# Optimization experiments

Hardware: AMD Instinct MI355X
Metric: run time of the kernel (lower is better)

## Reference

```python
import jax, jax.numpy as jnp
import numpy as np
from jax import lax


def setup_inputs() -> dict:
    key = jax.random.key(0)
    k1, k2, k3, k4, k5 = jax.random.split(key, 5)
    B, T, V, E, U = 64, 256, 32000, 256, 1024
    x = jax.random.randint(k1, (B, T), 0, V)          # token ids; 0 = pad (mask_zero=True)
    hidden = jnp.zeros((B, U), dtype=jnp.float32)      # initialize_hidden_state()
    emb = jax.random.normal(k2, (V, E), dtype=jnp.float32) * 0.05
    W = jax.random.normal(k3, (E, 3 * U), dtype=jnp.float32) * 0.05   # input kernel [z|r|h]
    Uk = jax.random.normal(k4, (U, 3 * U), dtype=jnp.float32) * 0.05  # recurrent kernel
    b = jax.random.normal(k5, (2, 3 * U), dtype=jnp.float32) * 0.05   # [input_bias, recurrent_bias] (reset_after=True)
    return {"x": x, "hidden": hidden, "emb": emb, "W": W, "U": Uk, "b": b}


def reference(x, hidden, emb, W, U, b):
    # Embedding with mask_zero=True: mask out pad tokens in the GRU scan.
    mask = (x != 0)                              # [B, T] bool
    xe = emb[x]                                  # [B, T, E]
    # Precompute all input projections in one big GEMM.
    xproj = jnp.einsum("bte,eu->btu", xe, W) + b[0]   # [B, T, 3U]
    nU = U.shape[0]

    def step(h, inp):
        xp, m = inp                              # xp: [B, 3U], m: [B]
        rec = h @ U + b[1]                       # [B, 3U]
        xz, xr, xh = jnp.split(xp, 3, axis=-1)
        rz, rr, rh = jnp.split(rec, 3, axis=-1)
        z = jax.nn.sigmoid(xz + rz)
        r = jax.nn.sigmoid(xr + rr)
        hh = jnp.tanh(xh + r * rh)               # reset_after=True form
        h_new = z * h + (1.0 - z) * hh
        h_new = jnp.where(m[:, None], h_new, h)  # masked steps carry state/output through
        return h_new, h_new

    state, outs = lax.scan(step, hidden,
                           (jnp.swapaxes(xproj, 0, 1), jnp.swapaxes(mask, 0, 1)))
    output = jnp.swapaxes(outs, 0, 1)            # [B, T, U]
    return output, state
```

## Files before the change

kernel.cpp:

```cpp
#include <hip/hip_runtime.h>
#include <hip/hip_cooperative_groups.h>

#define BB 64
#define TT 256
#define EE 256
#define NU 1024
#define N3 3072

typedef __attribute__((ext_vector_type(8))) short bf16x8;
typedef __attribute__((ext_vector_type(4))) float f32x4;

__device__ __forceinline__ unsigned short f2bf(float f) {
    unsigned u = __float_as_uint(f);
    return (unsigned short)((u + 0x7FFFu + ((u >> 16) & 1u)) >> 16);
}

__global__ __launch_bounds__(256) void upack_kernel(
    const float* __restrict__ U, float* __restrict__ up)
{
    __shared__ float t32[32][33];
    const int c0 = blockIdx.x * 32, k0 = blockIdx.y * 32;
    const int tx = threadIdx.x & 31, ty = threadIdx.x >> 5;
    #pragma unroll
    for (int i = 0; i < 4; ++i) {
        int k = ty + i * 8;
        t32[k][tx] = U[(size_t)(k0 + k) * N3 + c0 + tx];
    }
    __syncthreads();
    #pragma unroll
    for (int i = 0; i < 4; ++i) {
        int cl = ty + i * 8;
        int c = c0 + cl;
        int u = c & 1023, g = c >> 10;
        up[(size_t)(u * 3 + g) * NU + k0 + tx] = t32[tx][cl];
    }
}

__global__ __launch_bounds__(64) void tokT_kernel(
    const int* __restrict__ x, int* __restrict__ xT)
{
    const int t = blockIdx.x, b = threadIdx.x;
    xT[t * BB + b] = x[b * TT + t];
}

__global__ __launch_bounds__(256) void hinit_kernel(
    const float* __restrict__ hidden, unsigned short* __restrict__ hb0,
    unsigned* __restrict__ cnt)
{
    const int u = blockIdx.x * 4 + (threadIdx.x >> 6);
    const int b = threadIdx.x & 63;
    hb0[((u >> 3) * 64 + b) * 8 + (u & 7)] = f2bf(hidden[(size_t)b * NU + u]);
    if (blockIdx.x == 0) {
        cnt[threadIdx.x] = 0u;
        cnt[threadIdx.x + 256] = 0u;
    }
}

__global__ __launch_bounds__(256) void xprojT_kernel(
    const int* __restrict__ x, const float* __restrict__ emb,
    const float* __restrict__ W, const float* __restrict__ bias,
    float* __restrict__ xpT)
{
    __shared__ float AsT[32][132];
    __shared__ float Ws[32][132];
    __shared__ int toks[128];

    const int tid = threadIdx.x;
    const int mt = blockIdx.x / 24, nt = blockIdx.x % 24;
    const int m0 = mt * 128, n0 = nt * 128;

    if (tid < 128) {
        int mg = m0 + tid;
        toks[tid] = x[(mg & 63) * TT + (mg >> 6)];
    }
    __syncthreads();

    const int tx = tid & 15, ty = tid >> 4;
    float acc[8][8] = {};

    for (int kb = 0; kb < 8; ++kb) {
        const int k0 = kb * 32;
        if (kb) __syncthreads();
        #pragma unroll
        for (int i = 0; i < 4; ++i) {
            int idx = tid + 256 * i;
            int m = idx >> 3, c4 = idx & 7;
            float4 av = *(const float4*)(emb + (size_t)toks[m] * EE + k0 + c4 * 4);
            AsT[c4 * 4 + 0][m] = av.x; AsT[c4 * 4 + 1][m] = av.y;
            AsT[c4 * 4 + 2][m] = av.z; AsT[c4 * 4 + 3][m] = av.w;
            int r = idx >> 5, w4 = idx & 31;
            *(float4*)&Ws[r][w4 * 4] =
                *(const float4*)(W + (size_t)(k0 + r) * N3 + n0 + w4 * 4);
        }
        __syncthreads();
        #pragma unroll 8
        for (int kk = 0; kk < 32; ++kk) {
            float a8[8], w8[8];
            *(float4*)a8       = *(const float4*)&AsT[kk][ty * 8];
            *(float4*)(a8 + 4) = *(const float4*)&AsT[kk][ty * 8 + 4];
            *(float4*)w8       = *(const float4*)&Ws[kk][tx * 8];
            *(float4*)(w8 + 4) = *(const float4*)&Ws[kk][tx * 8 + 4];
            #pragma unroll
            for (int i = 0; i < 8; ++i)
                #pragma unroll
                for (int j = 0; j < 8; ++j) acc[i][j] += a8[i] * w8[j];
        }
    }

    float b8[8];
    *(float4*)b8       = *(const float4*)(bias + n0 + tx * 8);
    *(float4*)(b8 + 4) = *(const float4*)(bias + n0 + tx * 8 + 4);
    const int t0 = mt * 2 + (ty >> 3);
    const int bb0 = (ty & 7) * 8;
    #pragma unroll
    for (int j = 0; j < 8; ++j) {
        const int c = n0 + tx * 8 + j;
        float4 lo, hi;
        lo.x = acc[0][j] + b8[j]; lo.y = acc[1][j] + b8[j];
        lo.z = acc[2][j] + b8[j]; lo.w = acc[3][j] + b8[j];
        hi.x = acc[4][j] + b8[j]; hi.y = acc[5][j] + b8[j];
        hi.z = acc[6][j] + b8[j]; hi.w = acc[7][j] + b8[j];
        size_t base = ((size_t)t0 * N3 + c) * BB + bb0;
        *(float4*)(xpT + base)     = lo;
        *(float4*)(xpT + base + 4) = hi;
    }
}

__global__ __launch_bounds__(512) void gru_persist(
    const int* __restrict__ xT, const float* __restrict__ upack,
    const float* __restrict__ bias, float* xpT,
    float* __restrict__ out, const float* __restrict__ hidden,
    unsigned short* hb0, unsigned short* hb1, unsigned* cnt)
{
    __shared__ f32x4 red2[6144];
    __shared__ f32x4 redS[768];
    __shared__ unsigned short hstage[64 * 20];

    const int tid = threadIdx.x;
    const int U0 = blockIdx.x * 16;
    const int w = tid >> 6;
    const int lane = tid & 63;

    const int gdu = tid >> 5;
    const int gbA = tid & 31;

    bf16x8 af[3][4];
    {
        const int du = lane & 15;
        #pragma unroll
        for (int g = 0; g < 3; ++g)
            #pragma unroll
            for (int s = 0; s < 4; ++s) {
                const int k0 = w * 128 + s * 32 + (lane >> 4) * 8;
                const float* p = upack + (size_t)((U0 + du) * 3 + g) * NU + k0;
                float4 v0 = *(const float4*)p;
                float4 v1 = *(const float4*)(p + 4);
                af[g][s] = (bf16x8){ (short)f2bf(v0.x), (short)f2bf(v0.y),
                                     (short)f2bf(v0.z), (short)f2bf(v0.w),
                                     (short)f2bf(v1.x), (short)f2bf(v1.y),
                                     (short)f2bf(v1.z), (short)f2bf(v1.w) };
            }
    }

    float holdA = hidden[(size_t)gbA * NU + U0 + gdu];
    float holdB = hidden[(size_t)(gbA + 32) * NU + U0 + gdu];
    const float brz = bias[N3 + 0 * NU + U0 + gdu];
    const float brr = bias[N3 + 1 * NU + U0 + gdu];
    const float brh = bias[N3 + 2 * NU + U0 + gdu];
    float xzA, xrA, xhA, xzB, xrB, xhB; int tokA, tokB;
    {
        size_t xb = ((size_t)0 * N3 + U0 + gdu) * BB + gbA;
        xzA = xpT[xb];                      xzB = xpT[xb + 32];
        xrA = xpT[xb + (size_t)NU * BB];    xrB = xpT[xb + (size_t)NU * BB + 32];
        xhA = xpT[xb + (size_t)2 * NU * BB];xhB = xpT[xb + (size_t)2 * NU * BB + 32];
        tokA = xT[0 * BB + gbA];            tokB = xT[0 * BB + gbA + 32];
    }
    float* state_out = out + (size_t)BB * TT * NU;
    __syncthreads();

    const unsigned short* hc = hb0;
    unsigned short* hn = hb1;

    for (int t = 0; t < TT; ++t) {
        if (t > 0) {
            size_t ob = ((size_t)(t - 1) * N3 + U0 + gdu) * BB + gbA;
            __hip_atomic_store(&xpT[ob], holdA,
                               __ATOMIC_RELAXED, __HIP_MEMORY_SCOPE_SYSTEM);
            __hip_atomic_store(&xpT[ob + 32], holdB,
                               __ATOMIC_RELAXED, __HIP_MEMORY_SCOPE_SYSTEM);
        }

        bf16x8 bv[4][4];
        #pragma unroll
        for (int n = 0; n < 4; ++n)
            #pragma unroll
            for (int s = 0; s < 4; ++s) {
                const int ew = w * 16 + s * 4 + (lane >> 4);
                const unsigned long long* hq = (const unsigned long long*)(hc +
                    (size_t)(ew * 64 + n * 16 + (lane & 15)) * 8);
                union { unsigned long long q[2]; bf16x8 v; } uu;
                uu.q[0] = __hip_atomic_load(hq, __ATOMIC_RELAXED,
                                            __HIP_MEMORY_SCOPE_SYSTEM);
                uu.q[1] = __hip_atomic_load(hq + 1, __ATOMIC_RELAXED,
                                            __HIP_MEMORY_SCOPE_SYSTEM);
                bv[n][s] = uu.v;
            }

        f32x4 c[3][4];
        #pragma unroll
        for (int g = 0; g < 3; ++g)
            #pragma unroll
            for (int n = 0; n < 4; ++n) c[g][n] = (f32x4){0.f, 0.f, 0.f, 0.f};
        #pragma unroll
        for (int s = 0; s < 4; ++s)
            #pragma unroll
            for (int g = 0; g < 3; ++g)
                #pragma unroll
                for (int n = 0; n < 4; ++n)
                    c[g][n] = __builtin_amdgcn_mfma_f32_16x16x32_bf16(
                        af[g][s], bv[n][s], c[g][n], 0, 0, 0);

        #pragma unroll
        for (int g = 0; g < 3; ++g)
            #pragma unroll
            for (int n = 0; n < 4; ++n)
                red2[(w * 12 + g * 4 + n) * 64 + lane] = c[g][n];
        __syncthreads();

        {
            f32x4 s0 = red2[tid];
            #pragma unroll
            for (int q = 1; q < 8; ++q) s0 += red2[q * 768 + tid];
            redS[tid] = s0;
            if (tid < 256) {
                const int o2 = 512 + tid;
                f32x4 s1 = red2[o2];
                #pragma unroll
                for (int q = 1; q < 8; ++q) s1 += red2[q * 768 + o2];
                redS[o2] = s1;
            }
        }
        __syncthreads();

        {
            const int lA = (gdu >> 2) * 16 + (gbA & 15);
            const int rsub = gdu & 3;
            const int nA = gbA >> 4;
            float rzA = brz + ((const float*)&redS[(0 * 4 + nA) * 64 + lA])[rsub];
            float rrA = brr + ((const float*)&redS[(1 * 4 + nA) * 64 + lA])[rsub];
            float rhA = brh + ((const float*)&redS[(2 * 4 + nA) * 64 + lA])[rsub];
            float rzB = brz + ((const float*)&redS[(0 * 4 + nA + 2) * 64 + lA])[rsub];
            float rrB = brr + ((const float*)&redS[(1 * 4 + nA + 2) * 64 + lA])[rsub];
            float rhB = brh + ((const float*)&redS[(2 * 4 + nA + 2) * 64 + lA])[rsub];

            float zA  = 1.f / (1.f + expf(-(xzA + rzA)));
            float rA  = 1.f / (1.f + expf(-(xrA + rrA)));
            float hhA = tanhf(xhA + rA * rhA);
            float hnewA = zA * holdA + (1.f - zA) * hhA;
            if (tokA == 0) hnewA = holdA;
            float zB  = 1.f / (1.f + expf(-(xzB + rzB)));
            float rB  = 1.f / (1.f + expf(-(xrB + rrB)));
            float hhB = tanhf(xhB + rB * rhB);
            float hnewB = zB * holdB + (1.f - zB) * hhB;
            if (tokB == 0) hnewB = holdB;

            hstage[gbA * 20 + gdu] = f2bf(hnewA);
            hstage[(gbA + 32) * 20 + gdu] = f2bf(hnewB);
            holdA = hnewA; holdB = hnewB;
        }
        __syncthreads();

        if (w == 4 || w == 5) {
            const int g2 = w - 4;
            unsigned long long lo =
                *(const unsigned long long*)&hstage[lane * 20 + 8 * g2];
            unsigned long long hi =
                *(const unsigned long long*)&hstage[lane * 20 + 8 * g2 + 4];
            unsigned short* dst = hn + ((size_t)((U0 >> 3) + g2) * 64 + lane) * 8;
            __hip_atomic_store((unsigned long long*)dst, lo,
                               __ATOMIC_RELAXED, __HIP_MEMORY_SCOPE_SYSTEM);
            __hip_atomic_store((unsigned long long*)(dst + 4), hi,
                               __ATOMIC_RELAXED, __HIP_MEMORY_SCOPE_SYSTEM);
        }

        __builtin_amdgcn_s_waitcnt(0);
        __syncthreads();

        if (t + 1 < TT) {
            size_t xb = ((size_t)(t + 1) * N3 + U0 + gdu) * BB + gbA;
            xzA = xpT[xb];                      xzB = xpT[xb + 32];
            xrA = xpT[xb + (size_t)NU * BB];    xrB = xpT[xb + (size_t)NU * BB + 32];
            xhA = xpT[xb + (size_t)2 * NU * BB];xhB = xpT[xb + (size_t)2 * NU * BB + 32];
            tokA = xT[(t + 1) * BB + gbA];      tokB = xT[(t + 1) * BB + gbA + 32];
        }

        if (tid == 0) {
            const unsigned g = (unsigned)blockIdx.x >> 3;
            __hip_atomic_fetch_add(&cnt[g * 32], 1u,
                                   __ATOMIC_RELAXED, __HIP_MEMORY_SCOPE_SYSTEM);
            const unsigned tgt = 8u * ((unsigned)t + 1u);
            unsigned mn;
            long guard = 0;
            do {
                mn = 0xffffffffu;
                #pragma unroll
                for (int g8 = 0; g8 < 8; ++g8) {
                    unsigned v = __hip_atomic_load(&cnt[g8 * 32],
                                  __ATOMIC_RELAXED, __HIP_MEMORY_SCOPE_SYSTEM);
                    mn = v < mn ? v : mn;
                }
                if (mn < tgt) __builtin_amdgcn_s_sleep(1);
            } while (mn < tgt && ++guard < (1L << 24));
        }
        __syncthreads();

        const unsigned short* tmp = hc; hc = hn; hn = (unsigned short*)tmp;
    }

    {
        size_t ob = ((size_t)(TT - 1) * N3 + U0 + gdu) * BB + gbA;
        __hip_atomic_store(&xpT[ob], holdA,
                           __ATOMIC_RELAXED, __HIP_MEMORY_SCOPE_SYSTEM);
        __hip_atomic_store(&xpT[ob + 32], holdB,
                           __ATOMIC_RELAXED, __HIP_MEMORY_SCOPE_SYSTEM);
        __hip_atomic_store(&state_out[(size_t)gbA * NU + U0 + gdu], holdA,
                           __ATOMIC_RELAXED, __HIP_MEMORY_SCOPE_SYSTEM);
        __hip_atomic_store(&state_out[(size_t)(gbA + 32) * NU + U0 + gdu], holdB,
                           __ATOMIC_RELAXED, __HIP_MEMORY_SCOPE_SYSTEM);
    }
}

__global__ __launch_bounds__(256) void outT_kernel(
    const float* __restrict__ xpT, float* __restrict__ out)
{
    __shared__ float tile[64][65];
    const int t = blockIdx.x, u0 = blockIdx.y * 64;
    const int lane = threadIdx.x & 63, row = threadIdx.x >> 6;
    #pragma unroll
    for (int r = row; r < 64; r += 4)
        tile[r][lane] = xpT[((size_t)t * N3 + u0 + r) * BB + lane];
    __syncthreads();
    #pragma unroll
    for (int b = row; b < 64; b += 4)
        out[((size_t)b * TT + t) * NU + u0 + lane] = tile[lane][b];
}

extern "C" void kernel_launch(void* const* d_in, const int* in_sizes, int n_in,
                              void* d_out, int out_size, void* d_ws, size_t ws_size,
                              hipStream_t stream) {
    const int*   x      = (const int*)d_in[0];
    const float* hidden = (const float*)d_in[1];
    const float* emb    = (const float*)d_in[2];
    const float* W      = (const float*)d_in[3];
    const float* U      = (const float*)d_in[4];
    const float* bvec   = (const float*)d_in[5];

    float* out = (float*)d_out;

    float*          xpT   = (float*)d_ws;
    float*          upck  = xpT + (size_t)16384 * N3;
    unsigned short* hb0   = (unsigned short*)(upck + (size_t)3 * NU * NU);
    unsigned short* hb1   = hb0 + (size_t)NU * BB;
    int*            xT    = (int*)(hb1 + (size_t)NU * BB);
    unsigned*       cnt   = (unsigned*)(xT + TT * BB);

    upack_kernel<<<dim3(96, 32), dim3(256), 0, stream>>>(U, upck);
    tokT_kernel<<<dim3(TT), dim3(64), 0, stream>>>(x, xT);
    hinit_kernel<<<dim3(256), dim3(256), 0, stream>>>(hidden, hb0, cnt);
    xprojT_kernel<<<dim3(3072), dim3(256), 0, stream>>>(x, emb, W, bvec, xpT);

    void* args[] = {(void*)&xT, (void*)&upck, (void*)&bvec, (void*)&xpT,
                    (void*)&out, (void*)&hidden, (void*)&hb0, (void*)&hb1,
                    (void*)&cnt};
    hipLaunchCooperativeKernel((const void*)gru_persist, dim3(64), dim3(512),
                               args, 0, stream);

    outT_kernel<<<dim3(TT, 16), dim3(256), 0, stream>>>(xpT, out);
}
```

Measured before the change: 2.135 ms.

## Overlap input-projection GEMM with GRU recurrence inside the persistent kernel

The separate embedding/input-projection GEMM kernel is folded into the cooperative launch as 192 extra producer blocks. These compute xproj tiles and publish per-time-tile ready counters, which the 64 recurrence blocks poll before loading each step's inputs. The recurrence now writes hidden outputs straight into the final output layout, which removes the xpT round trip and the trailing transpose kernel. Producer blocks then spin on FMA busy-work until the recurrence finishes. The risks are uncoalesced output stores, flag polling on the critical path, and clock or power effects from the spinning blocks.

```diff
diff --git a/kernel.cpp b/kernel.cpp
--- a/kernel.cpp
+++ b/kernel.cpp
@@ -13,6 +13,11 @@
 __device__ __forceinline__ unsigned short f2bf(float f) {
     unsigned u = __float_as_uint(f);
     return (unsigned short)((u + 0x7FFFu + ((u >> 16) & 1u)) >> 16);
+}
+
+__device__ __forceinline__ unsigned long long packf2(float a, float b) {
+    return (unsigned long long)__float_as_uint(a) |
+           ((unsigned long long)__float_as_uint(b) << 32);
 }
 
 __global__ __launch_bounds__(256) void upack_kernel(
@@ -56,91 +61,124 @@
     }
 }
 
-__global__ __launch_bounds__(256) void xprojT_kernel(
-    const int* __restrict__ x, const float* __restrict__ emb,
-    const float* __restrict__ W, const float* __restrict__ bias,
-    float* __restrict__ xpT)
-{
-    __shared__ float AsT[32][132];
-    __shared__ float Ws[32][132];
-    __shared__ int toks[128];
-
-    const int tid = threadIdx.x;
-    const int mt = blockIdx.x / 24, nt = blockIdx.x % 24;
-    const int m0 = mt * 128, n0 = nt * 128;
-
-    if (tid < 128) {
-        int mg = m0 + tid;
-        toks[tid] = x[(mg & 63) * TT + (mg >> 6)];
-    }
-    __syncthreads();
-
-    const int tx = tid & 15, ty = tid >> 4;
-    float acc[8][8] = {};
-
-    for (int kb = 0; kb < 8; ++kb) {
-        const int k0 = kb * 32;
-        if (kb) __syncthreads();
-        #pragma unroll
-        for (int i = 0; i < 4; ++i) {
-            int idx = tid + 256 * i;
-            int m = idx >> 3, c4 = idx & 7;
-            float4 av = *(const float4*)(emb + (size_t)toks[m] * EE + k0 + c4 * 4);
-            AsT[c4 * 4 + 0][m] = av.x; AsT[c4 * 4 + 1][m] = av.y;
-            AsT[c4 * 4 + 2][m] = av.z; AsT[c4 * 4 + 3][m] = av.w;
-            int r = idx >> 5, w4 = idx & 31;
-            *(float4*)&Ws[r][w4 * 4] =
-                *(const float4*)(W + (size_t)(k0 + r) * N3 + n0 + w4 * 4);
-        }
-        __syncthreads();
-        #pragma unroll 8
-        for (int kk = 0; kk < 32; ++kk) {
-            float a8[8], w8[8];
-            *(float4*)a8       = *(const float4*)&AsT[kk][ty * 8];
-            *(float4*)(a8 + 4) = *(const float4*)&AsT[kk][ty * 8 + 4];
-            *(float4*)w8       = *(const float4*)&Ws[kk][tx * 8];
-            *(float4*)(w8 + 4) = *(const float4*)&Ws[kk][tx * 8 + 4];
-            #pragma unroll
-            for (int i = 0; i < 8; ++i)
-                #pragma unroll
-                for (int j = 0; j < 8; ++j) acc[i][j] += a8[i] * w8[j];
-        }
-    }
-
-    float b8[8];
-    *(float4*)b8       = *(const float4*)(bias + n0 + tx * 8);
-    *(float4*)(b8 + 4) = *(const float4*)(bias + n0 + tx * 8 + 4);
-    const int t0 = mt * 2 + (ty >> 3);
-    const int bb0 = (ty & 7) * 8;
-    #pragma unroll
-    for (int j = 0; j < 8; ++j) {
-        const int c = n0 + tx * 8 + j;
-        float4 lo, hi;
-        lo.x = acc[0][j] + b8[j]; lo.y = acc[1][j] + b8[j];
-        lo.z = acc[2][j] + b8[j]; lo.w = acc[3][j] + b8[j];
-        hi.x = acc[4][j] + b8[j]; hi.y = acc[5][j] + b8[j];
-        hi.z = acc[6][j] + b8[j]; hi.w = acc[7][j] + b8[j];
-        size_t base = ((size_t)t0 * N3 + c) * BB + bb0;
-        *(float4*)(xpT + base)     = lo;
-        *(float4*)(xpT + base + 4) = hi;
-    }
-}
-
 __global__ __launch_bounds__(512) void gru_persist(
     const int* __restrict__ xT, const float* __restrict__ upack,
     const float* __restrict__ bias, float* xpT,
     float* __restrict__ out, const float* __restrict__ hidden,
-    unsigned short* hb0, unsigned short* hb1, unsigned* cnt)
+    unsigned short* hb0, unsigned short* hb1, unsigned* cnt,
+    const int* __restrict__ x, const float* __restrict__ emb,
+    const float* __restrict__ W)
 {
     __shared__ f32x4 red2[6144];
     __shared__ f32x4 redS[768];
     __shared__ unsigned short hstage[64 * 20];
 
     const int tid = threadIdx.x;
+    unsigned* rdy = cnt + 320;
+
+    if (blockIdx.x >= 64) {
+        const int wid = blockIdx.x - 64;
+        float* AsT = (float*)red2;
+        float* Ws  = (float*)red2 + 4224;
+        int*  toks = (int*)((float*)red2 + 8448);
+        const int tx = tid & 15, ty2 = tid >> 4;
+
+        for (int idx0 = wid; idx0 < 3072; idx0 += 192) {
+            const int mt = idx0 / 24, nt = idx0 % 24;
+            const int m0 = mt * 128, n0 = nt * 128;
+
+            if (tid < 128) {
+                int mg = m0 + tid;
+                toks[tid] = x[(mg & 63) * TT + (mg >> 6)];
+            }
+            __syncthreads();
+
+            float acc[4][8] = {};
+            for (int kb = 0; kb < 8; ++kb) {
+                const int k0 = kb * 32;
+                if (kb) __syncthreads();
+                #pragma unroll
+                for (int i = 0; i < 2; ++i) {
+                    int idx = tid + 512 * i;
+                    int m = idx >> 3, c4 = idx & 7;
+                    float4 av = *(const float4*)(emb +
+                        (size_t)toks[m] * EE + k0 + c4 * 4);
+                    AsT[(c4 * 4 + 0) * 132 + m] = av.x;
+                    AsT[(c4 * 4 + 1) * 132 + m] = av.y;
+                    AsT[(c4 * 4 + 2) * 132 + m] = av.z;
+                    AsT[(c4 * 4 + 3) * 132 + m] = av.w;
+                    int r = idx >> 5, w4 = idx & 31;
+                    *(float4*)&Ws[r * 132 + w4 * 4] =
+                        *(const float4*)(W + (size_t)(k0 + r) * N3 + n0 + w4 * 4);
+                }
+                __syncthreads();
+                #pragma unroll 8
+                for (int kk = 0; kk < 32; ++kk) {
+                    float a4[4], w8[8];
+                    *(float4*)a4       = *(const float4*)&AsT[kk * 132 + ty2 * 4];
+                    *(float4*)w8       = *(const float4*)&Ws[kk * 132 + tx * 8];
+                    *(float4*)(w8 + 4) = *(const float4*)&Ws[kk * 132 + tx * 8 + 4];
+                    #pragma unroll
+                    for (int i = 0; i < 4; ++i)
+                        #pragma unroll
+                        for (int j = 0; j < 8; ++j) acc[i][j] += a4[i] * w8[j];
+                }
+            }
+
+            float b8[8];
+            *(float4*)b8       = *(const float4*)(bias + n0 + tx * 8);
+            *(float4*)(b8 + 4) = *(const float4*)(bias + n0 + tx * 8 + 4);
+            const int t0 = mt * 2 + (ty2 >> 4);
+            const int bq0 = (ty2 & 15) * 4;
+            #pragma unroll
+            for (int j = 0; j < 8; ++j) {
+                const int c = n0 + tx * 8 + j;
+                float f0 = acc[0][j] + b8[j], f1 = acc[1][j] + b8[j];
+                float f2 = acc[2][j] + b8[j], f3 = acc[3][j] + b8[j];
+                size_t base = ((size_t)t0 * N3 + c) * BB + bq0;
+                __hip_atomic_store((unsigned long long*)(xpT + base),
+                                   packf2(f0, f1),
+                                   __ATOMIC_RELAXED, __HIP_MEMORY_SCOPE_SYSTEM);
+                __hip_atomic_store((unsigned long long*)(xpT + base + 2),
+                                   packf2(f2, f3),
+                                   __ATOMIC_RELAXED, __HIP_MEMORY_SCOPE_SYSTEM);
+            }
+            __builtin_amdgcn_s_waitcnt(0);
+            __syncthreads();
+            if (tid == 0)
+                __hip_atomic_fetch_add(&rdy[mt], 1u,
+                                       __ATOMIC_RELAXED, __HIP_MEMORY_SCOPE_SYSTEM);
+            __syncthreads();
+        }
+
+        {
+            float d0 = 1.0f + tid * 1e-7f, d1 = 1.1f, d2 = 1.2f, d3 = 1.3f;
+            long guard = 0;
+            for (;;) {
+                unsigned mn = 0xffffffffu;
+                #pragma unroll
+                for (int g8 = 0; g8 < 8; ++g8) {
+                    unsigned v = __hip_atomic_load(&cnt[g8 * 32],
+                                  __ATOMIC_RELAXED, __HIP_MEMORY_SCOPE_SYSTEM);
+                    mn = v < mn ? v : mn;
+                }
+                if (mn >= 8u * TT || ++guard > (1L << 22)) break;
+                #pragma unroll
+                for (int d = 0; d < 256; ++d) {
+                    d0 = fmaf(d0, 1.0000001f, 1e-30f);
+                    d1 = fmaf(d1, 0.9999999f, 1e-30f);
+                    d2 = fmaf(d2, 1.0000002f, -1e-30f);
+                    d3 = fmaf(d3, 0.9999998f, -1e-30f);
+                }
+            }
+            asm volatile("" :: "v"(d0), "v"(d1), "v"(d2), "v"(d3));
+        }
+        return;
+    }
+
     const int U0 = blockIdx.x * 16;
     const int w = tid >> 6;
     const int lane = tid & 63;
-
     const int gdu = tid >> 5;
     const int gbA = tid & 31;
 
@@ -167,6 +205,15 @@
     const float brz = bias[N3 + 0 * NU + U0 + gdu];
     const float brr = bias[N3 + 1 * NU + U0 + gdu];
     const float brh = bias[N3 + 2 * NU + U0 + gdu];
+
+    {
+        unsigned r; long guard = 0;
+        do {
+            r = __hip_atomic_load(&rdy[0], __ATOMIC_RELAXED,
+                                  __HIP_MEMORY_SCOPE_SYSTEM);
+            if (r < 24u) __builtin_amdgcn_s_sleep(1);
+        } while (r < 24u && ++guard < (1L << 24));
+    }
     float xzA, xrA, xhA, xzB, xrB, xhB; int tokA, tokB;
     {
         size_t xb = ((size_t)0 * N3 + U0 + gdu) * BB + gbA;
@@ -183,11 +230,8 @@
 
     for (int t = 0; t < TT; ++t) {
         if (t > 0) {
-            size_t ob = ((size_t)(t - 1) * N3 + U0 + gdu) * BB + gbA;
-            __hip_atomic_store(&xpT[ob], holdA,
-                               __ATOMIC_RELAXED, __HIP_MEMORY_SCOPE_SYSTEM);
-            __hip_atomic_store(&xpT[ob + 32], holdB,
-                               __ATOMIC_RELAXED, __HIP_MEMORY_SCOPE_SYSTEM);
+            out[((size_t)gbA * TT + (t - 1)) * NU + U0 + gdu] = holdA;
+            out[((size_t)(gbA + 32) * TT + (t - 1)) * NU + U0 + gdu] = holdB;
         }
 
         bf16x8 bv[4][4];
@@ -287,6 +331,13 @@
         __syncthreads();
 
         if (t + 1 < TT) {
+            const int mtp = (t + 1) >> 1;
+            unsigned r; long guard = 0;
+            do {
+                r = __hip_atomic_load(&rdy[mtp], __ATOMIC_RELAXED,
+                                      __HIP_MEMORY_SCOPE_SYSTEM);
+                if (r < 24u) __builtin_amdgcn_s_sleep(1);
+            } while (r < 24u && ++guard < (1L << 24));
             size_t xb = ((size_t)(t + 1) * N3 + U0 + gdu) * BB + gbA;
             xzA = xpT[xb];                      xzB = xpT[xb + 32];
             xrA = xpT[xb + (size_t)NU * BB];    xrB = xpT[xb + (size_t)NU * BB + 32];
@@ -318,31 +369,11 @@
     }
 
     {
-        size_t ob = ((size_t)(TT - 1) * N3 + U0 + gdu) * BB + gbA;
-        __hip_atomic_store(&xpT[ob], holdA,
-                           __ATOMIC_RELAXED, __HIP_MEMORY_SCOPE_SYSTEM);
-        __hip_atomic_store(&xpT[ob + 32], holdB,
-                           __ATOMIC_RELAXED, __HIP_MEMORY_SCOPE_SYSTEM);
-        __hip_atomic_store(&state_out[(size_t)gbA * NU + U0 + gdu], holdA,
-                           __ATOMIC_RELAXED, __HIP_MEMORY_SCOPE_SYSTEM);
-        __hip_atomic_store(&state_out[(size_t)(gbA + 32) * NU + U0 + gdu], holdB,
-                           __ATOMIC_RELAXED, __HIP_MEMORY_SCOPE_SYSTEM);
-    }
-}
-
-__global__ __launch_bounds__(256) void outT_kernel(
-    const float* __restrict__ xpT, float* __restrict__ out)
-{
-    __shared__ float tile[64][65];
-    const int t = blockIdx.x, u0 = blockIdx.y * 64;
-    const int lane = threadIdx.x & 63, row = threadIdx.x >> 6;
-    #pragma unroll
-    for (int r = row; r < 64; r += 4)
-        tile[r][lane] = xpT[((size_t)t * N3 + u0 + r) * BB + lane];
-    __syncthreads();
-    #pragma unroll
-    for (int b = row; b < 64; b += 4)
-        out[((size_t)b * TT + t) * NU + u0 + lane] = tile[lane][b];
+        out[((size_t)gbA * TT + (TT - 1)) * NU + U0 + gdu] = holdA;
+        out[((size_t)(gbA + 32) * TT + (TT - 1)) * NU + U0 + gdu] = holdB;
+        state_out[(size_t)gbA * NU + U0 + gdu] = holdA;
+        state_out[(size_t)(gbA + 32) * NU + U0 + gdu] = holdB;
+    }
 }
 
 extern "C" void kernel_launch(void* const* d_in, const int* in_sizes, int n_in,
@@ -367,13 +398,10 @@
     upack_kernel<<<dim3(96, 32), dim3(256), 0, stream>>>(U, upck);
     tokT_kernel<<<dim3(TT), dim3(64), 0, stream>>>(x, xT);
     hinit_kernel<<<dim3(256), dim3(256), 0, stream>>>(hidden, hb0, cnt);
-    xprojT_kernel<<<dim3(3072), dim3(256), 0, stream>>>(x, emb, W, bvec, xpT);
 
     void* args[] = {(void*)&xT, (void*)&upck, (void*)&bvec, (void*)&xpT,
                     (void*)&out, (void*)&hidden, (void*)&hb0, (void*)&hb1,
-                    (void*)&cnt};
-    hipLaunchCooperativeKernel((const void*)gru_persist, dim3(64), dim3(512),
+                    (void*)&cnt, (void*)&x, (void*)&emb, (void*)&W};
+    hipLaunchCooperativeKernel((const void*)gru_persist, dim3(256), dim3(512),
                                args, 0, stream);
-
-    outT_kernel<<<dim3(TT, 16), dim3(256), 0, stream>>>(xpT, out);
-}
+}
```

New measurement: 1.993 ms. 1.07x faster.
